# Performance work log

Measured on AMD Instinct MI355X. Metric: run time of the kernel, lower is better.

## Reference

```python
import jax, jax.numpy as jnp
import numpy as np

N = 50000   # nodes
E = 600000  # edges
D = 128     # in_channels == heads*hidden_channels
OUT = 64    # out_channels
L = 3       # local_layers
EPS = 1e-5  # BatchNorm eps


def setup_inputs() -> dict:
    key = jax.random.key(0)
    ks = jax.random.split(key, 10)
    s = 0.05
    x = jax.random.normal(ks[0], (N, D), jnp.float32)
    edge_index = jax.random.randint(ks[1], (2, E), 0, N, dtype=jnp.int32)
    Wg = jax.random.normal(ks[2], (L, D, D), jnp.float32) * s  # GCNConv weights
    bg = jnp.zeros((L, D), jnp.float32)                         # GCNConv biases
    Wl = jax.random.normal(ks[3], (L, D, D), jnp.float32) * s  # residual Linear weights
    bl = jax.random.normal(ks[4], (L, D), jnp.float32) * s
    gamma = jnp.ones((L, D), jnp.float32)                       # BN scale
    beta = jnp.zeros((L, D), jnp.float32)                       # BN shift
    Wp = jax.random.normal(ks[5], (D, OUT), jnp.float32) * s   # pred head
    bp = jnp.zeros((OUT,), jnp.float32)
    return {"x": x, "edge_index": edge_index, "Wg": Wg, "bg": bg,
            "Wl": Wl, "bl": bl, "gamma": gamma, "beta": beta,
            "Wp": Wp, "bp": bp}


def reference(x, edge_index, Wg, bg, Wl, bl, gamma, beta, Wp, bp):
    src, dst = edge_index[0], edge_index[1]
    # GCN symmetric normalization with self-loops (PyG gcn_norm):
    # deg computed on target (col) including self-loop.
    deg = jax.ops.segment_sum(jnp.ones((E,), x.dtype), dst, num_segments=N) + 1.0
    dinv = jax.lax.rsqrt(deg)                      # deg^{-1/2}, [N]
    enorm = dinv[src] * dinv[dst]                  # per-edge norm, [E]
    self_norm = (dinv * dinv)[:, None]             # deg^{-1} for self-loop, [N,1]

    h = x
    x_local = jnp.zeros((N, D), x.dtype)
    for i in range(L):
        hg = h @ Wg[i]                             # [N, D] transformed features
        # gather -> weight -> scatter-add (message passing) + self-loop term
        agg = jax.ops.segment_sum(hg[src] * enorm[:, None], dst, num_segments=N)
        conv = agg + hg * self_norm + bg[i]
        # residual linear
        h = conv + h @ Wl[i] + bl[i]
        # BatchNorm1d (training-mode batch statistics, biased var)
        mu = jnp.mean(h, axis=0)
        var = jnp.mean(jnp.square(h - mu), axis=0)
        h = (h - mu) * jax.lax.rsqrt(var + EPS) * gamma[i] + beta[i]
        h = jax.nn.relu(h)
        x_local = x_local + h                      # add_ accumulation
    return x_local @ Wp + bp
```

## Files before the change

### kernel.cpp

```cpp
#include <hip/hip_runtime.h>

#define D 128
#define OUTC 64
#define STATB 256
#define EC 256

typedef float floatx4 __attribute__((ext_vector_type(4)));
typedef short short8 __attribute__((ext_vector_type(8)));

__device__ inline unsigned short f2bf(float f) {
  unsigned int u = __float_as_uint(f);
  unsigned int r = (u + 0x7FFF + ((u >> 16) & 1)) >> 16;
  return (unsigned short)r;
}

__device__ inline int swz(int row, int k) { return row * 128 + (k ^ ((row & 7) << 3)); }

__global__ __launch_bounds__(256) void k_prepx(const float* __restrict__ x, unsigned short* __restrict__ xb, int total4) {
  int stride = gridDim.x * blockDim.x;
  for (int i = blockIdx.x * blockDim.x + threadIdx.x; i < total4; i += stride) {
    float4 v = ((const float4*)x)[i];
    ushort4 o;
    o.x = f2bf(v.x); o.y = f2bf(v.y); o.z = f2bf(v.z); o.w = f2bf(v.w);
    ((ushort4*)xb)[i] = o;
  }
}

__global__ __launch_bounds__(256) void k_prepw(const float* __restrict__ Wg, const float* __restrict__ Wl,
                                               const float* __restrict__ Wp,
                                               unsigned short* __restrict__ Wgt, unsigned short* __restrict__ Wlt,
                                               unsigned short* __restrict__ Wpt) {
  int u = blockIdx.x * 256 + threadIdx.x;
  const int W1 = 3 * D * D;
  if (u < W1) {
    int i = u / (D * D), rem = u % (D * D);
    int k = rem / D, n = rem % D;
    Wgt[i * D * D + n * D + k] = f2bf(Wg[u]);
  } else if (u < 2 * W1) {
    int v = u - W1;
    int i = v / (D * D), rem = v % (D * D);
    int k = rem / D, n = rem % D;
    Wlt[i * D * D + n * D + k] = f2bf(Wl[v]);
  } else if (u < 2 * W1 + D * OUTC) {
    int v = u - 2 * W1;
    int k = v / OUTC, n = v % OUTC;
    Wpt[n * D + k] = f2bf(Wp[v]);
  }
}


__global__ __launch_bounds__(256) void k_bh(const int* __restrict__ dst, int* __restrict__ bh,
                                            int E, int nbuk, int chk) {
  __shared__ int hist[256];
  int t = threadIdx.x, c = blockIdx.x;
  hist[t] = 0;
  __syncthreads();
  int s = c * chk, e = min(E, s + chk);
  for (int j = s + t; j < e; j += 256)
    atomicAdd(&hist[dst[j] >> 8], 1);
  __syncthreads();
  if (t < nbuk) bh[t * EC + c] = hist[t];
}

__device__ inline int block_scan4(int4 v, int t, int* total) {
  int s = v.x + v.y + v.z + v.w;
  int lane = t & 63, w = t >> 6;
  int incl = s;
  #pragma unroll
  for (int off = 1; off < 64; off <<= 1) {
    int nb = __shfl_up(incl, off);
    if (lane >= off) incl += nb;
  }
  __shared__ int wsum[4];
  if (lane == 63) wsum[w] = incl;
  __syncthreads();
  int woff = 0;
  #pragma unroll
  for (int k = 0; k < 3; ++k) if (w > k) woff += wsum[k];
  if (total) *total = wsum[0] + wsum[1] + wsum[2] + wsum[3];
  return woff + incl - s;
}

__global__ __launch_bounds__(256) void k_gscan1(int* __restrict__ arr, int* __restrict__ bsum, int n) {
  int t = threadIdx.x;
  int i0 = blockIdx.x * 1024 + t * 4;
  int4 v = make_int4(0, 0, 0, 0);
  if (i0 + 3 < n) v = *(const int4*)(arr + i0);
  else {
    if (i0 < n) v.x = arr[i0];
    if (i0 + 1 < n) v.y = arr[i0 + 1];
    if (i0 + 2 < n) v.z = arr[i0 + 2];
    if (i0 + 3 < n) v.w = arr[i0 + 3];
  }
  int total;
  int e = block_scan4(v, t, &total);
  if (i0 < n) {
    int4 o;
    o.x = e; o.y = e + v.x; o.z = o.y + v.y; o.w = o.z + v.z;
    if (i0 + 3 < n) *(int4*)(arr + i0) = o;
    else {
      arr[i0] = o.x;
      if (i0 + 1 < n) arr[i0 + 1] = o.y;
      if (i0 + 2 < n) arr[i0 + 2] = o.z;
    }
  }
  if (t == 0) bsum[blockIdx.x] = total;
}

__global__ __launch_bounds__(256) void k_gscan2(int* __restrict__ bsum, int nb) {
  int t = threadIdx.x;
  int i0 = t * 4;
  int4 v = make_int4(0, 0, 0, 0);
  if (i0 + 3 < nb) v = *(const int4*)(bsum + i0);
  else {
    if (i0 < nb) v.x = bsum[i0];
    if (i0 + 1 < nb) v.y = bsum[i0 + 1];
    if (i0 + 2 < nb) v.z = bsum[i0 + 2];
    if (i0 + 3 < nb) v.w = bsum[i0 + 3];
  }
  int e = block_scan4(v, t, nullptr);
  if (i0 < nb) {
    bsum[i0] = e;
    if (i0 + 1 < nb) bsum[i0 + 1] = e + v.x;
    if (i0 + 2 < nb) bsum[i0 + 2] = e + v.x + v.y;
    if (i0 + 3 < nb) bsum[i0 + 3] = e + v.x + v.y + v.z;
  }
}

__global__ __launch_bounds__(256) void k_gscan3(int* __restrict__ arr, const int* __restrict__ bsum, int n) {
  int i = blockIdx.x * 256 + threadIdx.x;
  if (i < n) arr[i] += bsum[i >> 10];
}

__global__ __launch_bounds__(256) void k_scatter(const int* __restrict__ src, const int* __restrict__ dst,
                                                 const int* __restrict__ bhs, int2* __restrict__ ebuk,
                                                 int E, int nbuk, int chk) {
  __shared__ int cur[256];
  int t = threadIdx.x, c = blockIdx.x;
  if (t < nbuk) cur[t] = bhs[t * EC + c];
  __syncthreads();
  int s = c * chk, e = min(E, s + chk);
  for (int j = s + t; j < e; j += 256) {
    int d = dst[j];
    int pos = atomicAdd(&cur[d >> 8], 1);
    ebuk[pos] = make_int2(src[j], d);
  }
}

__global__ __launch_bounds__(256) void k_csr(const int2* __restrict__ ebuk, const int* __restrict__ bhs,
                                             int* __restrict__ rowstart, int* __restrict__ csr,
                                             float* __restrict__ dinv, int E, int N, int nbuk) {
  __shared__ int cnt[256];
  __shared__ int wsum[4];
  int t = threadIdx.x, b = blockIdx.x;
  int s = bhs[b * EC];
  int e = (b + 1 < nbuk) ? bhs[(b + 1) * EC] : E;
  cnt[t] = 0;
  __syncthreads();
  for (int j = s + t; j < e; j += 256)
    atomicAdd(&cnt[ebuk[j].y & 255], 1);
  __syncthreads();
  int v = cnt[t];
  int lane = t & 63, w = t >> 6;
  int incl = v;
  #pragma unroll
  for (int off = 1; off < 64; off <<= 1) {
    int nb = __shfl_up(incl, off);
    if (lane >= off) incl += nb;
  }
  if (lane == 63) wsum[w] = incl;
  __syncthreads();
  int woff = 0;
  #pragma unroll
  for (int k = 0; k < 3; ++k) if (w > k) woff += wsum[k];
  int rs = s + woff + incl - v;
  int node = (b << 8) + t;
  __syncthreads();
  cnt[t] = rs;
  if (node < N) {
    rowstart[node] = rs;
    dinv[node] = rsqrtf((float)v + 1.0f);
  }
  if (node == 0) rowstart[N] = E;
  __syncthreads();
  for (int j = s + t; j < e; j += 256) {
    int2 ed = ebuk[j];
    int pos = atomicAdd(&cnt[ed.y & 255], 1);
    csr[pos] = ed.x;
  }
}

__global__ __launch_bounds__(256) void k_dual(const unsigned short* __restrict__ Ab,
                                              const unsigned short* __restrict__ Wgt,
                                              const unsigned short* __restrict__ Wlt,
                                              unsigned short* __restrict__ hg, float* __restrict__ hl, int M) {
  __shared__ unsigned short As[64 * 128];
  __shared__ unsigned short Bs[128 * 128];
  int tid = threadIdx.x;
  int row0 = blockIdx.x * 64;

  {
    int r = tid >> 2;
    int row = row0 + r;
    const unsigned short* src = Ab + (size_t)row * D;
    #pragma unroll
    for (int j = 0; j < 4; ++j) {
      int c = (tid & 3) + j * 4;
      short8 v = {0, 0, 0, 0, 0, 0, 0, 0};
      if (row < M) v = *(const short8*)(src + c * 8);
      *(short8*)&As[swz(r, c * 8)] = v;
    }
  }
  #pragma unroll
  for (int j = 0; j < 8; ++j) {
    int idx = tid + j * 256;
    int nr = idx >> 4, c = idx & 15;
    *(short8*)&Bs[swz(nr, c * 8)] = *(const short8*)(Wgt + nr * D + c * 8);
  }
  __syncthreads();

  int lane = tid & 63, w = tid >> 6;
  int lrow = lane & 15, lk = (lane >> 4) * 8;

  short8 af[4][4];
  #pragma unroll
  for (int m = 0; m < 4; ++m) {
    int ar = lrow + m * 16;
    #pragma unroll
    for (int kk = 0; kk < 4; ++kk)
      af[m][kk] = *(const short8*)&As[swz(ar, lk + kk * 32)];
  }

  {
    short8 bfg[2][4];
    #pragma unroll
    for (int n = 0; n < 2; ++n) {
      int br = w * 32 + n * 16 + lrow;
      #pragma unroll
      for (int kk = 0; kk < 4; ++kk)
        bfg[n][kk] = *(const short8*)&Bs[swz(br, lk + kk * 32)];
    }
    floatx4 acc[4][2];
    #pragma unroll
    for (int m = 0; m < 4; ++m)
      #pragma unroll
      for (int n = 0; n < 2; ++n)
        acc[m][n] = (floatx4)0.0f;
    #pragma unroll
    for (int kk = 0; kk < 4; ++kk)
      #pragma unroll
      for (int m = 0; m < 4; ++m)
        #pragma unroll
        for (int n = 0; n < 2; ++n)
          acc[m][n] = __builtin_amdgcn_mfma_f32_16x16x32_bf16(af[m][kk], bfg[n][kk], acc[m][n], 0, 0, 0);
    #pragma unroll
    for (int m = 0; m < 4; ++m)
      #pragma unroll
      for (int n = 0; n < 2; ++n) {
        int col = w * 32 + n * 16 + lrow;
        #pragma unroll
        for (int reg = 0; reg < 4; ++reg) {
          int row = row0 + m * 16 + (lane >> 4) * 4 + reg;
          if (row < M) hg[(size_t)row * D + col] = f2bf(acc[m][n][reg]);
        }
      }
  }
  __syncthreads();
  #pragma unroll
  for (int j = 0; j < 8; ++j) {
    int idx = tid + j * 256;
    int nr = idx >> 4, c = idx & 15;
    *(short8*)&Bs[swz(nr, c * 8)] = *(const short8*)(Wlt + nr * D + c * 8);
  }
  __syncthreads();
  {
    short8 bfl[2][4];
    #pragma unroll
    for (int n = 0; n < 2; ++n) {
      int br = w * 32 + n * 16 + lrow;
      #pragma unroll
      for (int kk = 0; kk < 4; ++kk)
        bfl[n][kk] = *(const short8*)&Bs[swz(br, lk + kk * 32)];
    }
    floatx4 acc[4][2];
    #pragma unroll
    for (int m = 0; m < 4; ++m)
      #pragma unroll
      for (int n = 0; n < 2; ++n)
        acc[m][n] = (floatx4)0.0f;
    #pragma unroll
    for (int kk = 0; kk < 4; ++kk)
      #pragma unroll
      for (int m = 0; m < 4; ++m)
        #pragma unroll
        for (int n = 0; n < 2; ++n)
          acc[m][n] = __builtin_amdgcn_mfma_f32_16x16x32_bf16(af[m][kk], bfl[n][kk], acc[m][n], 0, 0, 0);
    #pragma unroll
    for (int m = 0; m < 4; ++m)
      #pragma unroll
      for (int n = 0; n < 2; ++n) {
        int col = w * 32 + n * 16 + lrow;
        #pragma unroll
        for (int reg = 0; reg < 4; ++reg) {
          int row = row0 + m * 16 + (lane >> 4) * 4 + reg;
          if (row < M) hl[(size_t)row * D + col] = acc[m][n][reg];
        }
      }
  }
}

__global__ __launch_bounds__(256) void k_agg(const unsigned short* __restrict__ hg, float* __restrict__ pre,
                                             const int* __restrict__ rowstart, const int* __restrict__ csr,
                                             const float* __restrict__ dinv,
                                             const float* __restrict__ bg, const float* __restrict__ bl, int n) {
  int node = (int)((blockIdx.x * blockDim.x + threadIdx.x) >> 6);
  if (node >= n) return;
  int lane = threadIdx.x & 63;
  int s = rowstart[node], e = rowstart[node + 1];
  const unsigned int* base = (const unsigned int*)hg;
  float a0 = 0.f, a1 = 0.f, b0 = 0.f, b1 = 0.f;
  float c0 = 0.f, c1 = 0.f, d0 = 0.f, d1 = 0.f;
  int j = s;
  for (; j + 4 <= e; j += 4) {
    int sn0 = csr[j], sn1 = csr[j + 1], sn2 = csr[j + 2], sn3 = csr[j + 3];
    float w0 = dinv[sn0], w1 = dinv[sn1], w2 = dinv[sn2], w3 = dinv[sn3];
    unsigned int p0 = base[(size_t)sn0 * 64 + lane];
    unsigned int p1 = base[(size_t)sn1 * 64 + lane];
    unsigned int p2 = base[(size_t)sn2 * 64 + lane];
    unsigned int p3 = base[(size_t)sn3 * 64 + lane];
    a0 += w0 * __uint_as_float(p0 << 16); a1 += w0 * __uint_as_float(p0 & 0xFFFF0000u);
    b0 += w1 * __uint_as_float(p1 << 16); b1 += w1 * __uint_as_float(p1 & 0xFFFF0000u);
    c0 += w2 * __uint_as_float(p2 << 16); c1 += w2 * __uint_as_float(p2 & 0xFFFF0000u);
    d0 += w3 * __uint_as_float(p3 << 16); d1 += w3 * __uint_as_float(p3 & 0xFFFF0000u);
  }
  for (; j < e; ++j) {
    int sn = csr[j];
    float w = dinv[sn];
    unsigned int p = base[(size_t)sn * 64 + lane];
    a0 += w * __uint_as_float(p << 16);
    a1 += w * __uint_as_float(p & 0xFFFF0000u);
  }
  float acc0 = (a0 + b0) + (c0 + d0);
  float acc1 = (a1 + b1) + (c1 + d1);
  float dn = dinv[node];
  float sf = dn * dn;
  unsigned int ps = base[(size_t)node * 64 + lane];
  float h0 = __uint_as_float(ps << 16);
  float h1 = __uint_as_float(ps & 0xFFFF0000u);
  int c = lane * 2;
  float* pp = pre + (size_t)node * D;
  float2 old = *(const float2*)(pp + c);
  float p0 = dn * acc0 + h0 * sf + bg[c] + old.x + bl[c];
  float p1 = dn * acc1 + h1 * sf + bg[c + 1] + old.y + bl[c + 1];
  *(float2*)(pp + c) = make_float2(p0, p1);
}

__global__ __launch_bounds__(256) void k_stats(const float* __restrict__ pre, float* __restrict__ partial, int n) {
  int t = threadIdx.x;
  int c4 = t & 31;
  int rl = t >> 5;
  int r = blockIdx.x * 8 + rl;
  int rstride = gridDim.x * 8;
  float4 s = make_float4(0.f, 0.f, 0.f, 0.f), q = make_float4(0.f, 0.f, 0.f, 0.f);
  for (; r < n; r += rstride) {
    float4 v = *(const float4*)(pre + (size_t)r * D + c4 * 4);
    s.x += v.x; s.y += v.y; s.z += v.z; s.w += v.w;
    q.x += v.x * v.x; q.y += v.y * v.y; q.z += v.z * v.z; q.w += v.w * v.w;
  }
  __shared__ float4 ls[256], lq[256];
  ls[t] = s; lq[t] = q;
  __syncthreads();
  if (t < 32) {
    #pragma unroll
    for (int j = 1; j < 8; ++j) {
      float4 a = ls[t + j * 32], b = lq[t + j * 32];
      s.x += a.x; s.y += a.y; s.z += a.z; s.w += a.w;
      q.x += b.x; q.y += b.y; q.z += b.z; q.w += b.w;
    }
    int c = t * 4;
    int b = blockIdx.x;
    partial[(c + 0) * STATB + b] = s.x;
    partial[(c + 1) * STATB + b] = s.y;
    partial[(c + 2) * STATB + b] = s.z;
    partial[(c + 3) * STATB + b] = s.w;
    partial[(128 + c + 0) * STATB + b] = q.x;
    partial[(128 + c + 1) * STATB + b] = q.y;
    partial[(128 + c + 2) * STATB + b] = q.z;
    partial[(128 + c + 3) * STATB + b] = q.w;
  }
}

__global__ void k_finalize(const float* __restrict__ partial, const float* __restrict__ gamma,
                           const float* __restrict__ beta, float* __restrict__ ab, float invN) {
  int c = threadIdx.x;
  const float4* ps = (const float4*)(partial + (size_t)c * STATB);
  const float4* pq = (const float4*)(partial + (size_t)(128 + c) * STATB);
  float s = 0.f, q = 0.f;
  #pragma unroll 8
  for (int i = 0; i < STATB / 4; ++i) {
    float4 a = ps[i], b = pq[i];
    s += a.x + a.y + a.z + a.w;
    q += b.x + b.y + b.z + b.w;
  }
  float mean = s * invN;
  float var = q * invN - mean * mean;
  float inv = rsqrtf(var + 1e-5f);
  float g = gamma[c];
  ab[c] = g * inv;
  ab[128 + c] = beta[c] - mean * inv * g;
}

template<bool FIRST>
__global__ __launch_bounds__(256) void k_out(const float* __restrict__ pre, const float* __restrict__ ab,
                                             const unsigned short* __restrict__ Wpt, const float* __restrict__ bp,
                                             unsigned short* __restrict__ hb, float* __restrict__ out, int M) {
  __shared__ unsigned short As[64 * 128];
  __shared__ unsigned short Bs[OUTC * 128];
  int tid = threadIdx.x;
  int row0 = blockIdx.x * 64;

  {
    int r = tid >> 2, qq = tid & 3;
    int row = row0 + r;
    bool valid = row < M;
    const float* Pp = pre + (size_t)row * D;
    #pragma unroll
    for (int ch = 0; ch < 4; ++ch) {
      int k0 = qq * 32 + ch * 8;
      float4 p0 = make_float4(0.f, 0.f, 0.f, 0.f), p1 = p0;
      if (valid) { p0 = *(const float4*)(Pp + k0); p1 = *(const float4*)(Pp + k0 + 4); }
      float4 a0 = *(const float4*)(ab + k0),        a1 = *(const float4*)(ab + k0 + 4);
      float4 b0 = *(const float4*)(ab + 128 + k0),  b1 = *(const float4*)(ab + 128 + k0 + 4);
      unsigned short hv[8];
      hv[0] = f2bf(fmaxf(p0.x * a0.x + b0.x, 0.f));
      hv[1] = f2bf(fmaxf(p0.y * a0.y + b0.y, 0.f));
      hv[2] = f2bf(fmaxf(p0.z * a0.z + b0.z, 0.f));
      hv[3] = f2bf(fmaxf(p0.w * a0.w + b0.w, 0.f));
      hv[4] = f2bf(fmaxf(p1.x * a1.x + b1.x, 0.f));
      hv[5] = f2bf(fmaxf(p1.y * a1.y + b1.y, 0.f));
      hv[6] = f2bf(fmaxf(p1.z * a1.z + b1.z, 0.f));
      hv[7] = f2bf(fmaxf(p1.w * a1.w + b1.w, 0.f));
      short8 v = *(const short8*)hv;
      *(short8*)&As[swz(r, k0)] = v;
      if (valid) *(short8*)(hb + (size_t)row * D + k0) = v;
    }
  }
  #pragma unroll
  for (int j = 0; j < 4; ++j) {
    int idx = tid + j * 256;
    int nr = idx >> 4, c = idx & 15;
    *(short8*)&Bs[swz(nr, c * 8)] = *(const short8*)(Wpt + nr * D + c * 8);
  }
  __syncthreads();

  int lane = tid & 63, w = tid >> 6;
  int lrow = lane & 15, lk = (lane >> 4) * 8;

  short8 af[4][4];
  #pragma unroll
  for (int m = 0; m < 4; ++m) {
    int ar = lrow + m * 16;
    #pragma unroll
    for (int kk = 0; kk < 4; ++kk)
      af[m][kk] = *(const short8*)&As[swz(ar, lk + kk * 32)];
  }
  short8 bfr[4];
  {
    int br = w * 16 + lrow;
    #pragma unroll
    for (int kk = 0; kk < 4; ++kk)
      bfr[kk] = *(const short8*)&Bs[swz(br, lk + kk * 32)];
  }
  floatx4 acc[4];
  #pragma unroll
  for (int m = 0; m < 4; ++m) acc[m] = (floatx4)0.0f;
  #pragma unroll
  for (int kk = 0; kk < 4; ++kk)
    #pragma unroll
    for (int m = 0; m < 4; ++m)
      acc[m] = __builtin_amdgcn_mfma_f32_16x16x32_bf16(af[m][kk], bfr[kk], acc[m], 0, 0, 0);

  int col = w * 16 + lrow;
  float bpv = FIRST ? bp[col] : 0.f;
  #pragma unroll
  for (int m = 0; m < 4; ++m)
    #pragma unroll
    for (int reg = 0; reg < 4; ++reg) {
      int row = row0 + m * 16 + (lane >> 4) * 4 + reg;
      if (row < M) {
        float* op = &out[(size_t)row * OUTC + col];
        float v = acc[m][reg] + bpv;
        if (!FIRST) v += *op;
        *op = v;
      }
    }
}

extern "C" void kernel_launch(void* const* d_in, const int* in_sizes, int n_in,
                              void* d_out, int out_size, void* d_ws, size_t ws_size,
                              hipStream_t stream) {
  const float* x     = (const float*)d_in[0];
  const int*   ei    = (const int*)d_in[1];
  const float* Wg    = (const float*)d_in[2];
  const float* bg    = (const float*)d_in[3];
  const float* Wl    = (const float*)d_in[4];
  const float* bl    = (const float*)d_in[5];
  const float* gamma = (const float*)d_in[6];
  const float* beta  = (const float*)d_in[7];
  const float* Wp    = (const float*)d_in[8];
  const float* bp    = (const float*)d_in[9];
  float* out = (float*)d_out;

  int N = in_sizes[0] / D;
  int E = in_sizes[1] / 2;
  const int* srcp = ei;
  const int* dstp = ei + E;

  char* wsb = (char*)d_ws;
  size_t off = 0;
  auto alloc = [&](size_t bytes) {
    off = (off + 255) & ~(size_t)255;
    void* p = wsb + off;
    off += bytes;
    return p;
  };
  float* dinv     = (float*)alloc((size_t)N * 4);
  int*   rowstart = (int*)alloc((size_t)(N + 1) * 4);
  int*   csr      = (int*)alloc((size_t)E * 4);
  int*   bh       = (int*)alloc((size_t)256 * EC * 4);
  int2*  ebuk     = (int2*)alloc((size_t)E * 8);
  int*   bsum     = (int*)alloc(1024 * 4);
  float* partial  = (float*)alloc((size_t)256 * STATB * 4);
  float* ab       = (float*)alloc(3 * 256 * 4);
  unsigned short* xb  = (unsigned short*)alloc((size_t)N * D * 2);
  unsigned short* hb  = (unsigned short*)alloc((size_t)N * D * 2);
  unsigned short* hg  = (unsigned short*)alloc((size_t)N * D * 2);
  float* hl       = (float*)alloc((size_t)N * D * 4);
  unsigned short* Wgt = (unsigned short*)alloc(3 * D * D * 2);
  unsigned short* Wlt = (unsigned short*)alloc(3 * D * D * 2);
  unsigned short* Wpt = (unsigned short*)alloc(D * OUTC * 2);
  (void)ws_size; (void)n_in; (void)out_size;

  k_prepx<<<1024, 256, 0, stream>>>(x, xb, N * D / 4);
  int wtotal = 2 * 3 * D * D + D * OUTC;
  k_prepw<<<(wtotal + 255) / 256, 256, 0, stream>>>(Wg, Wl, Wp, Wgt, Wlt, Wpt);

  int nbuk = (N + 255) >> 8;
  int chk  = (E + EC - 1) / EC;
  k_bh<<<EC, 256, 0, stream>>>(dstp, bh, E, nbuk, chk);
  int sn  = nbuk * EC;
  int snb = (sn + 1023) >> 10;
  k_gscan1<<<snb, 256, 0, stream>>>(bh, bsum, sn);
  k_gscan2<<<1, 256, 0, stream>>>(bsum, snb);
  k_gscan3<<<(sn + 255) / 256, 256, 0, stream>>>(bh, bsum, sn);
  k_scatter<<<EC, 256, 0, stream>>>(srcp, dstp, bh, ebuk, E, nbuk, chk);
  k_csr<<<nbuk, 256, 0, stream>>>(ebuk, bh, rowstart, csr, dinv, E, N, nbuk);

  int mt = (N + 63) / 64;
  for (int i = 0; i < 3; ++i) {
    const unsigned short* A = (i == 0) ? xb : hb;
    k_dual<<<mt, 256, 0, stream>>>(A, Wgt + (size_t)i * D * D, Wlt + (size_t)i * D * D, hg, hl, N);
    k_agg<<<(N + 3) / 4, 256, 0, stream>>>(hg, hl, rowstart, csr, dinv, bg + (size_t)i * D, bl + (size_t)i * D, N);
    k_stats<<<STATB, 256, 0, stream>>>(hl, partial, N);
    k_finalize<<<1, 128, 0, stream>>>(partial, gamma + (size_t)i * D, beta + (size_t)i * D, ab + i * 256, 1.0f / (float)N);
    if (i == 0) k_out<true ><<<mt, 256, 0, stream>>>(hl, ab + i * 256, Wpt, bp, hb, out, N);
    else        k_out<false><<<mt, 256, 0, stream>>>(hl, ab + i * 256, Wpt, bp, hb, out, N);
  }
}
```

Measured before the change: 329.9 us.

## Fuse BN stats into aggregation and next-layer GEMMs into output projection

Folds the global-scan fixup into the scatter and CSR kernels, removing one launch. The aggregation kernel now accumulates per-block BatchNorm sums and sums of squares, which removes the separate stats pass over the fp32 pre-activation buffer. A new fused kernel applies BN+ReLU, does the output projection, and computes the next layer's Wg and Wl GEMMs from the same LDS tile. This avoids writing and re-reading the bf16 hidden buffer and drops the separate dual-GEMM launch. Biases move into the GEMM epilogue. The costs are a larger partial-stats buffer, a wider finalize kernel, and heavier fused kernels that need more LDS, which may lower occupancy.

```diff
diff --git a/kernel.cpp b/kernel.cpp
--- a/kernel.cpp
+++ b/kernel.cpp
@@ -2,7 +2,6 @@
 
 #define D 128
 #define OUTC 64
-#define STATB 256
 #define EC 256
 
 typedef float floatx4 __attribute__((ext_vector_type(4)));
@@ -127,17 +126,15 @@
   }
 }
 
-__global__ __launch_bounds__(256) void k_gscan3(int* __restrict__ arr, const int* __restrict__ bsum, int n) {
-  int i = blockIdx.x * 256 + threadIdx.x;
-  if (i < n) arr[i] += bsum[i >> 10];
-}
-
 __global__ __launch_bounds__(256) void k_scatter(const int* __restrict__ src, const int* __restrict__ dst,
-                                                 const int* __restrict__ bhs, int2* __restrict__ ebuk,
-                                                 int E, int nbuk, int chk) {
+                                                 const int* __restrict__ bhs, const int* __restrict__ bsum,
+                                                 int2* __restrict__ ebuk, int E, int nbuk, int chk) {
   __shared__ int cur[256];
   int t = threadIdx.x, c = blockIdx.x;
-  if (t < nbuk) cur[t] = bhs[t * EC + c];
+  if (t < nbuk) {
+    int idx = t * EC + c;
+    cur[t] = bhs[idx] + bsum[idx >> 10];
+  }
   __syncthreads();
   int s = c * chk, e = min(E, s + chk);
   for (int j = s + t; j < e; j += 256) {
@@ -148,13 +145,17 @@
 }
 
 __global__ __launch_bounds__(256) void k_csr(const int2* __restrict__ ebuk, const int* __restrict__ bhs,
+                                             const int* __restrict__ bsum,
                                              int* __restrict__ rowstart, int* __restrict__ csr,
                                              float* __restrict__ dinv, int E, int N, int nbuk) {
   __shared__ int cnt[256];
   __shared__ int wsum[4];
   int t = threadIdx.x, b = blockIdx.x;
-  int s = bhs[b * EC];
-  int e = (b + 1 < nbuk) ? bhs[(b + 1) * EC] : E;
+  int si = b * EC;
+  int s = bhs[si] + bsum[si >> 10];
+  int e;
+  if (b + 1 < nbuk) { int ei_ = (b + 1) * EC; e = bhs[ei_] + bsum[ei_ >> 10]; }
+  else e = E;
   cnt[t] = 0;
   __syncthreads();
   for (int j = s + t; j < e; j += 256)
@@ -193,6 +194,7 @@
 __global__ __launch_bounds__(256) void k_dual(const unsigned short* __restrict__ Ab,
                                               const unsigned short* __restrict__ Wgt,
                                               const unsigned short* __restrict__ Wlt,
+                                              const float* __restrict__ bg, const float* __restrict__ bl,
                                               unsigned short* __restrict__ hg, float* __restrict__ hl, int M) {
   __shared__ unsigned short As[64 * 128];
   __shared__ unsigned short Bs[128 * 128];
@@ -300,10 +302,11 @@
       #pragma unroll
       for (int n = 0; n < 2; ++n) {
         int col = w * 32 + n * 16 + lrow;
+        float bias = bg[col] + bl[col];
         #pragma unroll
         for (int reg = 0; reg < 4; ++reg) {
           int row = row0 + m * 16 + (lane >> 4) * 4 + reg;
-          if (row < M) hl[(size_t)row * D + col] = acc[m][n][reg];
+          if (row < M) hl[(size_t)row * D + col] = acc[m][n][reg] + bias;
         }
       }
   }
@@ -312,110 +315,108 @@
 __global__ __launch_bounds__(256) void k_agg(const unsigned short* __restrict__ hg, float* __restrict__ pre,
                                              const int* __restrict__ rowstart, const int* __restrict__ csr,
                                              const float* __restrict__ dinv,
-                                             const float* __restrict__ bg, const float* __restrict__ bl, int n) {
-  int node = (int)((blockIdx.x * blockDim.x + threadIdx.x) >> 6);
-  if (node >= n) return;
-  int lane = threadIdx.x & 63;
-  int s = rowstart[node], e = rowstart[node + 1];
+                                             float* __restrict__ partial, int n, int ABS) {
+  int t = threadIdx.x, b = blockIdx.x;
+  int w = t >> 6, lane = t & 63;
   const unsigned int* base = (const unsigned int*)hg;
-  float a0 = 0.f, a1 = 0.f, b0 = 0.f, b1 = 0.f;
-  float c0 = 0.f, c1 = 0.f, d0 = 0.f, d1 = 0.f;
-  int j = s;
-  for (; j + 4 <= e; j += 4) {
-    int sn0 = csr[j], sn1 = csr[j + 1], sn2 = csr[j + 2], sn3 = csr[j + 3];
-    float w0 = dinv[sn0], w1 = dinv[sn1], w2 = dinv[sn2], w3 = dinv[sn3];
-    unsigned int p0 = base[(size_t)sn0 * 64 + lane];
-    unsigned int p1 = base[(size_t)sn1 * 64 + lane];
-    unsigned int p2 = base[(size_t)sn2 * 64 + lane];
-    unsigned int p3 = base[(size_t)sn3 * 64 + lane];
-    a0 += w0 * __uint_as_float(p0 << 16); a1 += w0 * __uint_as_float(p0 & 0xFFFF0000u);
-    b0 += w1 * __uint_as_float(p1 << 16); b1 += w1 * __uint_as_float(p1 & 0xFFFF0000u);
-    c0 += w2 * __uint_as_float(p2 << 16); c1 += w2 * __uint_as_float(p2 & 0xFFFF0000u);
-    d0 += w3 * __uint_as_float(p3 << 16); d1 += w3 * __uint_as_float(p3 & 0xFFFF0000u);
-  }
-  for (; j < e; ++j) {
-    int sn = csr[j];
-    float w = dinv[sn];
-    unsigned int p = base[(size_t)sn * 64 + lane];
-    a0 += w * __uint_as_float(p << 16);
-    a1 += w * __uint_as_float(p & 0xFFFF0000u);
-  }
-  float acc0 = (a0 + b0) + (c0 + d0);
-  float acc1 = (a1 + b1) + (c1 + d1);
-  float dn = dinv[node];
-  float sf = dn * dn;
-  unsigned int ps = base[(size_t)node * 64 + lane];
-  float h0 = __uint_as_float(ps << 16);
-  float h1 = __uint_as_float(ps & 0xFFFF0000u);
+  float st_s0 = 0.f, st_s1 = 0.f, st_q0 = 0.f, st_q1 = 0.f;
   int c = lane * 2;
-  float* pp = pre + (size_t)node * D;
-  float2 old = *(const float2*)(pp + c);
-  float p0 = dn * acc0 + h0 * sf + bg[c] + old.x + bl[c];
-  float p1 = dn * acc1 + h1 * sf + bg[c + 1] + old.y + bl[c + 1];
-  *(float2*)(pp + c) = make_float2(p0, p1);
-}
-
-__global__ __launch_bounds__(256) void k_stats(const float* __restrict__ pre, float* __restrict__ partial, int n) {
+  int node0 = b * 16 + w * 4;
+  #pragma unroll 1
+  for (int k = 0; k < 4; ++k) {
+    int node = node0 + k;
+    if (node >= n) break;
+    int s = rowstart[node], e = rowstart[node + 1];
+    float dn = dinv[node];
+    unsigned int ps = base[(size_t)node * 64 + lane];
+    float* pp = pre + (size_t)node * D;
+    float2 old = *(const float2*)(pp + c);
+    float a0 = 0.f, a1 = 0.f, b0 = 0.f, b1 = 0.f;
+    float c0 = 0.f, c1 = 0.f, d0 = 0.f, d1 = 0.f;
+    int j = s;
+    for (; j + 4 <= e; j += 4) {
+      int sn0 = csr[j], sn1 = csr[j + 1], sn2 = csr[j + 2], sn3 = csr[j + 3];
+      float w0 = dinv[sn0], w1 = dinv[sn1], w2 = dinv[sn2], w3 = dinv[sn3];
+      unsigned int p0 = base[(size_t)sn0 * 64 + lane];
+      unsigned int p1 = base[(size_t)sn1 * 64 + lane];
+      unsigned int p2 = base[(size_t)sn2 * 64 + lane];
+      unsigned int p3 = base[(size_t)sn3 * 64 + lane];
+      a0 += w0 * __uint_as_float(p0 << 16); a1 += w0 * __uint_as_float(p0 & 0xFFFF0000u);
+      b0 += w1 * __uint_as_float(p1 << 16); b1 += w1 * __uint_as_float(p1 & 0xFFFF0000u);
+      c0 += w2 * __uint_as_float(p2 << 16); c1 += w2 * __uint_as_float(p2 & 0xFFFF0000u);
+      d0 += w3 * __uint_as_float(p3 << 16); d1 += w3 * __uint_as_float(p3 & 0xFFFF0000u);
+    }
+    for (; j < e; ++j) {
+      int sn = csr[j];
+      float wv = dinv[sn];
+      unsigned int p = base[(size_t)sn * 64 + lane];
+      a0 += wv * __uint_as_float(p << 16);
+      a1 += wv * __uint_as_float(p & 0xFFFF0000u);
+    }
+    float acc0 = (a0 + b0) + (c0 + d0);
+    float acc1 = (a1 + b1) + (c1 + d1);
+    float sf = dn * dn;
+    float h0 = __uint_as_float(ps << 16);
+    float h1 = __uint_as_float(ps & 0xFFFF0000u);
+    float p0 = dn * acc0 + h0 * sf + old.x;
+    float p1 = dn * acc1 + h1 * sf + old.y;
+    *(float2*)(pp + c) = make_float2(p0, p1);
+    st_s0 += p0; st_s1 += p1;
+    st_q0 += p0 * p0; st_q1 += p1 * p1;
+  }
+  __shared__ float sm[4][128], sq[4][128];
+  sm[w][c] = st_s0; sm[w][c + 1] = st_s1;
+  sq[w][c] = st_q0; sq[w][c + 1] = st_q1;
+  __syncthreads();
+  if (t < 128) {
+    float s = (sm[0][t] + sm[1][t]) + (sm[2][t] + sm[3][t]);
+    float q = (sq[0][t] + sq[1][t]) + (sq[2][t] + sq[3][t]);
+    partial[(size_t)t * ABS + b] = s;
+    partial[(size_t)(128 + t) * ABS + b] = q;
+  }
+}
+
+__global__ __launch_bounds__(256) void k_fin2(const float* __restrict__ partial,
+                                              const float* __restrict__ gamma, const float* __restrict__ beta,
+                                              float* __restrict__ ab, int nab, int ABS, float invN) {
+  int cch = blockIdx.x;
   int t = threadIdx.x;
-  int c4 = t & 31;
-  int rl = t >> 5;
-  int r = blockIdx.x * 8 + rl;
-  int rstride = gridDim.x * 8;
-  float4 s = make_float4(0.f, 0.f, 0.f, 0.f), q = make_float4(0.f, 0.f, 0.f, 0.f);
-  for (; r < n; r += rstride) {
-    float4 v = *(const float4*)(pre + (size_t)r * D + c4 * 4);
-    s.x += v.x; s.y += v.y; s.z += v.z; s.w += v.w;
-    q.x += v.x * v.x; q.y += v.y * v.y; q.z += v.z * v.z; q.w += v.w * v.w;
-  }
-  __shared__ float4 ls[256], lq[256];
-  ls[t] = s; lq[t] = q;
-  __syncthreads();
-  if (t < 32) {
-    #pragma unroll
-    for (int j = 1; j < 8; ++j) {
-      float4 a = ls[t + j * 32], b = lq[t + j * 32];
-      s.x += a.x; s.y += a.y; s.z += a.z; s.w += a.w;
-      q.x += b.x; q.y += b.y; q.z += b.z; q.w += b.w;
-    }
-    int c = t * 4;
-    int b = blockIdx.x;
-    partial[(c + 0) * STATB + b] = s.x;
-    partial[(c + 1) * STATB + b] = s.y;
-    partial[(c + 2) * STATB + b] = s.z;
-    partial[(c + 3) * STATB + b] = s.w;
-    partial[(128 + c + 0) * STATB + b] = q.x;
-    partial[(128 + c + 1) * STATB + b] = q.y;
-    partial[(128 + c + 2) * STATB + b] = q.z;
-    partial[(128 + c + 3) * STATB + b] = q.w;
-  }
-}
-
-__global__ void k_finalize(const float* __restrict__ partial, const float* __restrict__ gamma,
-                           const float* __restrict__ beta, float* __restrict__ ab, float invN) {
-  int c = threadIdx.x;
-  const float4* ps = (const float4*)(partial + (size_t)c * STATB);
-  const float4* pq = (const float4*)(partial + (size_t)(128 + c) * STATB);
+  const float* ps = partial + (size_t)cch * ABS;
+  const float* pq = partial + (size_t)(128 + cch) * ABS;
   float s = 0.f, q = 0.f;
-  #pragma unroll 8
-  for (int i = 0; i < STATB / 4; ++i) {
-    float4 a = ps[i], b = pq[i];
-    s += a.x + a.y + a.z + a.w;
-    q += b.x + b.y + b.z + b.w;
-  }
-  float mean = s * invN;
-  float var = q * invN - mean * mean;
-  float inv = rsqrtf(var + 1e-5f);
-  float g = gamma[c];
-  ab[c] = g * inv;
-  ab[128 + c] = beta[c] - mean * inv * g;
+  for (int i = t; i < nab; i += 256) { s += ps[i]; q += pq[i]; }
+  __shared__ float rs[256], rq[256];
+  rs[t] = s; rq[t] = q;
+  __syncthreads();
+  if (t < 64) {
+    s = (rs[t] + rs[t + 64]) + (rs[t + 128] + rs[t + 192]);
+    q = (rq[t] + rq[t + 64]) + (rq[t + 128] + rq[t + 192]);
+    #pragma unroll
+    for (int off = 32; off; off >>= 1) {
+      s += __shfl_down(s, off);
+      q += __shfl_down(q, off);
+    }
+    if (t == 0) {
+      float mean = s * invN;
+      float var = q * invN - mean * mean;
+      float inv = rsqrtf(var + 1e-5f);
+      float g = gamma[cch];
+      ab[cch] = g * inv;
+      ab[128 + cch] = beta[cch] - mean * inv * g;
+    }
+  }
 }
 
 template<bool FIRST>
-__global__ __launch_bounds__(256) void k_out(const float* __restrict__ pre, const float* __restrict__ ab,
-                                             const unsigned short* __restrict__ Wpt, const float* __restrict__ bp,
-                                             unsigned short* __restrict__ hb, float* __restrict__ out, int M) {
+__global__ __launch_bounds__(256) void k_fused(const float* __restrict__ pre, const float* __restrict__ ab,
+                                               const unsigned short* __restrict__ Wpt, const float* __restrict__ bp,
+                                               const unsigned short* __restrict__ Wgt,
+                                               const unsigned short* __restrict__ Wlt,
+                                               const float* __restrict__ bgn, const float* __restrict__ bln,
+                                               float* __restrict__ out, unsigned short* __restrict__ hg,
+                                               float* __restrict__ hl, int M) {
   __shared__ unsigned short As[64 * 128];
-  __shared__ unsigned short Bs[OUTC * 128];
+  __shared__ unsigned short Bs[128 * 128];
   int tid = threadIdx.x;
   int row0 = blockIdx.x * 64;
 
@@ -440,9 +441,7 @@
       hv[5] = f2bf(fmaxf(p1.y * a1.y + b1.y, 0.f));
       hv[6] = f2bf(fmaxf(p1.z * a1.z + b1.z, 0.f));
       hv[7] = f2bf(fmaxf(p1.w * a1.w + b1.w, 0.f));
-      short8 v = *(const short8*)hv;
-      *(short8*)&As[swz(r, k0)] = v;
-      if (valid) *(short8*)(hb + (size_t)row * D + k0) = v;
+      *(short8*)&As[swz(r, k0)] = *(const short8*)hv;
     }
   }
   #pragma unroll
@@ -464,6 +463,174 @@
     for (int kk = 0; kk < 4; ++kk)
       af[m][kk] = *(const short8*)&As[swz(ar, lk + kk * 32)];
   }
+
+  {
+    short8 bfr[4];
+    int br = w * 16 + lrow;
+    #pragma unroll
+    for (int kk = 0; kk < 4; ++kk)
+      bfr[kk] = *(const short8*)&Bs[swz(br, lk + kk * 32)];
+    floatx4 acc[4];
+    #pragma unroll
+    for (int m = 0; m < 4; ++m) acc[m] = (floatx4)0.0f;
+    #pragma unroll
+    for (int kk = 0; kk < 4; ++kk)
+      #pragma unroll
+      for (int m = 0; m < 4; ++m)
+        acc[m] = __builtin_amdgcn_mfma_f32_16x16x32_bf16(af[m][kk], bfr[kk], acc[m], 0, 0, 0);
+    int col = w * 16 + lrow;
+    float bpv = FIRST ? bp[col] : 0.f;
+    #pragma unroll
+    for (int m = 0; m < 4; ++m)
+      #pragma unroll
+      for (int reg = 0; reg < 4; ++reg) {
+        int row = row0 + m * 16 + (lane >> 4) * 4 + reg;
+        if (row < M) {
+          float* op = &out[(size_t)row * OUTC + col];
+          float v = acc[m][reg] + bpv;
+          if (!FIRST) v += *op;
+          *op = v;
+        }
+      }
+  }
+  __syncthreads();
+  #pragma unroll
+  for (int j = 0; j < 8; ++j) {
+    int idx = tid + j * 256;
+    int nr = idx >> 4, c = idx & 15;
+    *(short8*)&Bs[swz(nr, c * 8)] = *(const short8*)(Wgt + nr * D + c * 8);
+  }
+  __syncthreads();
+  {
+    short8 bfg[2][4];
+    #pragma unroll
+    for (int n = 0; n < 2; ++n) {
+      int br = w * 32 + n * 16 + lrow;
+      #pragma unroll
+      for (int kk = 0; kk < 4; ++kk)
+        bfg[n][kk] = *(const short8*)&Bs[swz(br, lk + kk * 32)];
+    }
+    floatx4 acc[4][2];
+    #pragma unroll
+    for (int m = 0; m < 4; ++m)
+      #pragma unroll
+      for (int n = 0; n < 2; ++n)
+        acc[m][n] = (floatx4)0.0f;
+    #pragma unroll
+    for (int kk = 0; kk < 4; ++kk)
+      #pragma unroll
+      for (int m = 0; m < 4; ++m)
+        #pragma unroll
+        for (int n = 0; n < 2; ++n)
+          acc[m][n] = __builtin_amdgcn_mfma_f32_16x16x32_bf16(af[m][kk], bfg[n][kk], acc[m][n], 0, 0, 0);
+    #pragma unroll
+    for (int m = 0; m < 4; ++m)
+      #pragma unroll
+      for (int n = 0; n < 2; ++n) {
+        int col = w * 32 + n * 16 + lrow;
+        #pragma unroll
+        for (int reg = 0; reg < 4; ++reg) {
+          int row = row0 + m * 16 + (lane >> 4) * 4 + reg;
+          if (row < M) hg[(size_t)row * D + col] = f2bf(acc[m][n][reg]);
+        }
+      }
+  }
+  __syncthreads();
+  #pragma unroll
+  for (int j = 0; j < 8; ++j) {
+    int idx = tid + j * 256;
+    int nr = idx >> 4, c = idx & 15;
+    *(short8*)&Bs[swz(nr, c * 8)] = *(const short8*)(Wlt + nr * D + c * 8);
+  }
+  __syncthreads();
+  {
+    short8 bfl[2][4];
+    #pragma unroll
+    for (int n = 0; n < 2; ++n) {
+      int br = w * 32 + n * 16 + lrow;
+      #pragma unroll
+      for (int kk = 0; kk < 4; ++kk)
+        bfl[n][kk] = *(const short8*)&Bs[swz(br, lk + kk * 32)];
+    }
+    floatx4 acc[4][2];
+    #pragma unroll
+    for (int m = 0; m < 4; ++m)
+      #pragma unroll
+      for (int n = 0; n < 2; ++n)
+        acc[m][n] = (floatx4)0.0f;
+    #pragma unroll
+    for (int kk = 0; kk < 4; ++kk)
+      #pragma unroll
+      for (int m = 0; m < 4; ++m)
+        #pragma unroll
+        for (int n = 0; n < 2; ++n)
+          acc[m][n] = __builtin_amdgcn_mfma_f32_16x16x32_bf16(af[m][kk], bfl[n][kk], acc[m][n], 0, 0, 0);
+    #pragma unroll
+    for (int m = 0; m < 4; ++m)
+      #pragma unroll
+      for (int n = 0; n < 2; ++n) {
+        int col = w * 32 + n * 16 + lrow;
+        float bias = bgn[col] + bln[col];
+        #pragma unroll
+        for (int reg = 0; reg < 4; ++reg) {
+          int row = row0 + m * 16 + (lane >> 4) * 4 + reg;
+          if (row < M) hl[(size_t)row * D + col] = acc[m][n][reg] + bias;
+        }
+      }
+  }
+}
+
+__global__ __launch_bounds__(256) void k_out(const float* __restrict__ pre, const float* __restrict__ ab,
+                                             const unsigned short* __restrict__ Wpt,
+                                             float* __restrict__ out, int M) {
+  __shared__ unsigned short As[64 * 128];
+  __shared__ unsigned short Bs[OUTC * 128];
+  int tid = threadIdx.x;
+  int row0 = blockIdx.x * 64;
+
+  {
+    int r = tid >> 2, qq = tid & 3;
+    int row = row0 + r;
+    bool valid = row < M;
+    const float* Pp = pre + (size_t)row * D;
+    #pragma unroll
+    for (int ch = 0; ch < 4; ++ch) {
+      int k0 = qq * 32 + ch * 8;
+      float4 p0 = make_float4(0.f, 0.f, 0.f, 0.f), p1 = p0;
+      if (valid) { p0 = *(const float4*)(Pp + k0); p1 = *(const float4*)(Pp + k0 + 4); }
+      float4 a0 = *(const float4*)(ab + k0),        a1 = *(const float4*)(ab + k0 + 4);
+      float4 b0 = *(const float4*)(ab + 128 + k0),  b1 = *(const float4*)(ab + 128 + k0 + 4);
+      unsigned short hv[8];
+      hv[0] = f2bf(fmaxf(p0.x * a0.x + b0.x, 0.f));
+      hv[1] = f2bf(fmaxf(p0.y * a0.y + b0.y, 0.f));
+      hv[2] = f2bf(fmaxf(p0.z * a0.z + b0.z, 0.f));
+      hv[3] = f2bf(fmaxf(p0.w * a0.w + b0.w, 0.f));
+      hv[4] = f2bf(fmaxf(p1.x * a1.x + b1.x, 0.f));
+      hv[5] = f2bf(fmaxf(p1.y * a1.y + b1.y, 0.f));
+      hv[6] = f2bf(fmaxf(p1.z * a1.z + b1.z, 0.f));
+      hv[7] = f2bf(fmaxf(p1.w * a1.w + b1.w, 0.f));
+      *(short8*)&As[swz(r, k0)] = *(const short8*)hv;
+    }
+  }
+  #pragma unroll
+  for (int j = 0; j < 4; ++j) {
+    int idx = tid + j * 256;
+    int nr = idx >> 4, c = idx & 15;
+    *(short8*)&Bs[swz(nr, c * 8)] = *(const short8*)(Wpt + nr * D + c * 8);
+  }
+  __syncthreads();
+
+  int lane = tid & 63, w = tid >> 6;
+  int lrow = lane & 15, lk = (lane >> 4) * 8;
+
+  short8 af[4][4];
+  #pragma unroll
+  for (int m = 0; m < 4; ++m) {
+    int ar = lrow + m * 16;
+    #pragma unroll
+    for (int kk = 0; kk < 4; ++kk)
+      af[m][kk] = *(const short8*)&As[swz(ar, lk + kk * 32)];
+  }
   short8 bfr[4];
   {
     int br = w * 16 + lrow;
@@ -481,7 +648,6 @@
       acc[m] = __builtin_amdgcn_mfma_f32_16x16x32_bf16(af[m][kk], bfr[kk], acc[m], 0, 0, 0);
 
   int col = w * 16 + lrow;
-  float bpv = FIRST ? bp[col] : 0.f;
   #pragma unroll
   for (int m = 0; m < 4; ++m)
     #pragma unroll
@@ -489,9 +655,7 @@
       int row = row0 + m * 16 + (lane >> 4) * 4 + reg;
       if (row < M) {
         float* op = &out[(size_t)row * OUTC + col];
-        float v = acc[m][reg] + bpv;
-        if (!FIRST) v += *op;
-        *op = v;
+        *op = *op + acc[m][reg];
       }
     }
 }
@@ -524,16 +688,17 @@
     off += bytes;
     return p;
   };
+  int nab = (N + 15) / 16;
+  int ABS = (nab + 63) & ~63;
   float* dinv     = (float*)alloc((size_t)N * 4);
   int*   rowstart = (int*)alloc((size_t)(N + 1) * 4);
   int*   csr      = (int*)alloc((size_t)E * 4);
   int*   bh       = (int*)alloc((size_t)256 * EC * 4);
   int2*  ebuk     = (int2*)alloc((size_t)E * 8);
   int*   bsum     = (int*)alloc(1024 * 4);
-  float* partial  = (float*)alloc((size_t)256 * STATB * 4);
+  float* partial  = (float*)alloc((size_t)256 * ABS * 4);
   float* ab       = (float*)alloc(3 * 256 * 4);
   unsigned short* xb  = (unsigned short*)alloc((size_t)N * D * 2);
-  unsigned short* hb  = (unsigned short*)alloc((size_t)N * D * 2);
   unsigned short* hg  = (unsigned short*)alloc((size_t)N * D * 2);
   float* hl       = (float*)alloc((size_t)N * D * 4);
   unsigned short* Wgt = (unsigned short*)alloc(3 * D * D * 2);
@@ -552,18 +717,29 @@
   int snb = (sn + 1023) >> 10;
   k_gscan1<<<snb, 256, 0, stream>>>(bh, bsum, sn);
   k_gscan2<<<1, 256, 0, stream>>>(bsum, snb);
-  k_gscan3<<<(sn + 255) / 256, 256, 0, stream>>>(bh, bsum, sn);
-  k_scatter<<<EC, 256, 0, stream>>>(srcp, dstp, bh, ebuk, E, nbuk, chk);
-  k_csr<<<nbuk, 256, 0, stream>>>(ebuk, bh, rowstart, csr, dinv, E, N, nbuk);
+  k_scatter<<<EC, 256, 0, stream>>>(srcp, dstp, bh, bsum, ebuk, E, nbuk, chk);
+  k_csr<<<nbuk, 256, 0, stream>>>(ebuk, bh, bsum, rowstart, csr, dinv, E, N, nbuk);
 
   int mt = (N + 63) / 64;
+  float invN = 1.0f / (float)N;
+
+  k_dual<<<mt, 256, 0, stream>>>(xb, Wgt, Wlt, bg, bl, hg, hl, N);
+
   for (int i = 0; i < 3; ++i) {
-    const unsigned short* A = (i == 0) ? xb : hb;
-    k_dual<<<mt, 256, 0, stream>>>(A, Wgt + (size_t)i * D * D, Wlt + (size_t)i * D * D, hg, hl, N);
-    k_agg<<<(N + 3) / 4, 256, 0, stream>>>(hg, hl, rowstart, csr, dinv, bg + (size_t)i * D, bl + (size_t)i * D, N);
-    k_stats<<<STATB, 256, 0, stream>>>(hl, partial, N);
-    k_finalize<<<1, 128, 0, stream>>>(partial, gamma + (size_t)i * D, beta + (size_t)i * D, ab + i * 256, 1.0f / (float)N);
-    if (i == 0) k_out<true ><<<mt, 256, 0, stream>>>(hl, ab + i * 256, Wpt, bp, hb, out, N);
-    else        k_out<false><<<mt, 256, 0, stream>>>(hl, ab + i * 256, Wpt, bp, hb, out, N);
-  }
-}
+    k_agg<<<nab, 256, 0, stream>>>(hg, hl, rowstart, csr, dinv, partial, N, ABS);
+    k_fin2<<<128, 256, 0, stream>>>(partial, gamma + (size_t)i * D, beta + (size_t)i * D,
+                                    ab + i * 256, nab, ABS, invN);
+    if (i == 0)
+      k_fused<true><<<mt, 256, 0, stream>>>(hl, ab + i * 256, Wpt, bp,
+                                            Wgt + (size_t)(i + 1) * D * D, Wlt + (size_t)(i + 1) * D * D,
+                                            bg + (size_t)(i + 1) * D, bl + (size_t)(i + 1) * D,
+                                            out, hg, hl, N);
+    else if (i == 1)
+      k_fused<false><<<mt, 256, 0, stream>>>(hl, ab + i * 256, Wpt, bp,
+                                             Wgt + (size_t)(i + 1) * D * D, Wlt + (size_t)(i + 1) * D * D,
+                                             bg + (size_t)(i + 1) * D, bl + (size_t)(i + 1) * D,
+                                             out, hg, hl, N);
+    else
+      k_out<<<mt, 256, 0, stream>>>(hl, ab + i * 256, Wpt, out, N);
+  }
+}
```

New measurement: 290.8 us. 1.13x faster.
